# Kernel tuning notes

Measured on AMD Instinct MI355X. Metric: run time of the kernel, lower is better.

Reference implementation:

```python
import jax, jax.numpy as jnp
import numpy as np

EPS = 1e-8

def setup_inputs() -> dict:
    key = jax.random.key(0)
    k1, k2, k3, k4 = jax.random.split(key, 4)
    B, S, K, N = 8, 32, 8192, 8192
    x = jax.random.normal(k1, (B, S, K), dtype=jnp.float32)
    # unpacked AWQ 4-bit weights: int8 values in [-8, 7] (stored as int32 here)
    qweight = jax.random.randint(k2, (K, N), -8, 8, dtype=jnp.int32)
    w_scales = jax.random.uniform(k3, (N,), dtype=jnp.float32) * 0.01 + 1e-4
    bias = jax.random.normal(k4, (N,), dtype=jnp.float32)
    return {"x": x, "qweight": qweight, "w_scales": w_scales, "bias": bias}

def reference(x, qweight, w_scales, bias):
    K = x.shape[-1]
    x2 = x.reshape(-1, K)                                  # [M, K]
    # per-token symmetric int8 activation quantization
    max_abs = jnp.max(jnp.abs(x2), axis=-1, keepdims=True)  # [M, 1]
    act_scales = jnp.maximum(max_abs / 127.0, EPS)
    x_q = jnp.clip(jnp.round(x2 / act_scales), -127, 127).astype(jnp.int8)
    out = x_q.astype(jnp.float32) @ qweight.astype(jnp.float32)  # [M, N]
    # dequant rescale: per-token * per-channel, then bias
    out = out * act_scales * w_scales[None, :] + bias[None, :]
    out = out.reshape(*x.shape[:-1], out.shape[-1])
    return out.astype(x.dtype)
```

## Files before the change

### kernel.cpp

```cpp
#include <hip/hip_runtime.h>

#define M_ 256
#define K_ 8192
#define N_ 8192

typedef int v4i __attribute__((ext_vector_type(4)));
typedef int v16i __attribute__((ext_vector_type(16)));

__global__ __launch_bounds__(256) void awq_quant(const float* __restrict__ x,
                                                 signed char* __restrict__ xqt,
                                                 float* __restrict__ scales) {
    const int m = blockIdx.x;
    const int t = threadIdx.x;
    const float4* xrow = (const float4*)(x + (size_t)m * K_);
    float4 v[8];
    float mx = 0.0f;
#pragma unroll
    for (int j = 0; j < 8; ++j) {
        v[j] = xrow[j * 256 + t];
        mx = fmaxf(mx, fmaxf(fmaxf(fabsf(v[j].x), fabsf(v[j].y)),
                             fmaxf(fabsf(v[j].z), fabsf(v[j].w))));
    }
#pragma unroll
    for (int off = 32; off > 0; off >>= 1) mx = fmaxf(mx, __shfl_xor(mx, off, 64));
    __shared__ float red[4];
    if ((t & 63) == 0) red[t >> 6] = mx;
    __syncthreads();
    mx = fmaxf(fmaxf(red[0], red[1]), fmaxf(red[2], red[3]));
    const float scale = fmaxf(mx / 127.0f, 1e-8f);

    char* base = (char*)xqt + ((size_t)(m >> 5) << 18);
    const int ml = m & 31;
#pragma unroll
    for (int j = 0; j < 8; ++j) {
        const int q0 = (int)fminf(fmaxf(rintf(v[j].x / scale), -127.0f), 127.0f);
        const int q1 = (int)fminf(fmaxf(rintf(v[j].y / scale), -127.0f), 127.0f);
        const int q2 = (int)fminf(fmaxf(rintf(v[j].z / scale), -127.0f), 127.0f);
        const int q3 = (int)fminf(fmaxf(rintf(v[j].w / scale), -127.0f), 127.0f);
        const int packed = (q0 & 255) | ((q1 & 255) << 8) | ((q2 & 255) << 16) | ((q3 & 255) << 24);
        const int k0 = 4 * (j * 256 + t);
        const int addr = ((k0 >> 8) << 13) + (((k0 >> 5) & 7) << 10) +
                         ((ml + (((k0 >> 4) & 1) << 5)) << 4) + (k0 & 15);
        *(int*)(base + addr) = packed;
    }
    if (t == 0) scales[m] = scale;
}


__device__ __forceinline__ void stage_b(char* btn, int bwo,
                                        const int4& w0, const int4& w1,
                                        const int4& w2, const int4& w3) {
    const int* p0 = (const int*)&w0;
    const int* p1 = (const int*)&w1;
    const int* p2 = (const int*)&w2;
    const int* p3 = (const int*)&w3;
#pragma unroll
    for (int j = 0; j < 4; ++j) {
        const unsigned u = __builtin_amdgcn_perm((unsigned)p1[j], (unsigned)p0[j], 0x00000400u);
        const unsigned w = __builtin_amdgcn_perm((unsigned)p3[j], (unsigned)p2[j], 0x00000400u);
        const unsigned o = __builtin_amdgcn_perm(w, u, 0x05040100u);
        *(unsigned*)(btn + bwo + j * 272) = o;
    }
}

__global__ __launch_bounds__(512) void awq_gemm(const signed char* __restrict__ xqt,
                                                const float* __restrict__ scales,
                                                const int* __restrict__ qw,
                                                const float* __restrict__ wscale,
                                                const float* __restrict__ bias,
                                                float* __restrict__ out) {
    __shared__ __align__(16) char btile[2][32 * 272];
    const int t = threadIdx.x;
    const int lane = t & 63;
    const int wave = t >> 6;
    const int n0 = blockIdx.x * 32;

    const int sa = t & 7;
    const int sr = t >> 3;
    const int* qbase = qw + (size_t)(4 * sr) * N_ + n0 + 4 * sa;

    const signed char* xqb = xqt + ((size_t)wave << 18) + lane * 16;

    const int bro = (lane & 31) * 272 + (lane >> 5) * 16;
    const int bwo = (4 * sa) * 272 + 4 * sr;

    v16i acc = {};
    v4i aE[8], aO[8];
    int4 sA[4], sB[4];

    auto loadq = [&](int4* dst, int chunk) {
        const int4* q = (const int4*)(qbase + (size_t)chunk * 256 * N_);
        dst[0] = q[0];
        dst[1] = q[N_ / 4];
        dst[2] = q[2 * (N_ / 4)];
        dst[3] = q[3 * (N_ / 4)];
    };

#pragma unroll
    for (int ks = 0; ks < 8; ++ks) aE[ks] = *(const v4i*)(xqb + ks * 1024);
    loadq(sA, 0);
    loadq(sB, 1);
    stage_b(&btile[0][0], bwo, sA[0], sA[1], sA[2], sA[3]);
    asm volatile("s_waitcnt lgkmcnt(0)" ::: "memory");
    __builtin_amdgcn_s_barrier();
    __builtin_amdgcn_sched_barrier(0);

    for (int sc = 0; sc < 32; sc += 2) {
        {
            const int ra = (sc + 1 < 32) ? sc + 1 : 31;
#pragma unroll
            for (int ks = 0; ks < 8; ++ks)
                aO[ks] = *(const v4i*)(xqb + ra * 8192 + ks * 1024);
            const int c2 = (sc + 2 < 32) ? sc + 2 : 31;
            loadq(sA, c2);
            __builtin_amdgcn_sched_barrier(0);
            const char* btc = &btile[0][0];
#pragma unroll
            for (int ks = 0; ks < 8; ++ks) {
                const v4i bf = *(const v4i*)(btc + bro + ks * 32);
                acc = __builtin_amdgcn_mfma_i32_32x32x32_i8(aE[ks], bf, acc, 0, 0, 0);
            }
            stage_b(&btile[1][0], bwo, sB[0], sB[1], sB[2], sB[3]);
            asm volatile("s_waitcnt lgkmcnt(0)" ::: "memory");
            __builtin_amdgcn_s_barrier();
            __builtin_amdgcn_sched_barrier(0);
        }
        {
            const int ra = (sc + 2 < 32) ? sc + 2 : 31;
#pragma unroll
            for (int ks = 0; ks < 8; ++ks)
                aE[ks] = *(const v4i*)(xqb + ra * 8192 + ks * 1024);
            const int c3 = (sc + 3 < 32) ? sc + 3 : 31;
            loadq(sB, c3);
            __builtin_amdgcn_sched_barrier(0);
            const char* btc = &btile[1][0];
#pragma unroll
            for (int ks = 0; ks < 8; ++ks) {
                const v4i bf = *(const v4i*)(btc + bro + ks * 32);
                acc = __builtin_amdgcn_mfma_i32_32x32x32_i8(aO[ks], bf, acc, 0, 0, 0);
            }
            stage_b(&btile[0][0], bwo, sA[0], sA[1], sA[2], sA[3]);
            asm volatile("s_waitcnt lgkmcnt(0)" ::: "memory");
            __builtin_amdgcn_s_barrier();
            __builtin_amdgcn_sched_barrier(0);
        }
    }

    const int n = n0 + (lane & 31);
    const float wn = wscale[n];
    const float bn = bias[n];
    const int mb = wave * 32 + 4 * (lane >> 5);
#pragma unroll
    for (int g = 0; g < 16; ++g) {
        const int m = mb + (g & 3) + 8 * (g >> 2);
        out[(size_t)m * N_ + n] = ((float)acc[g] * scales[m]) * wn + bn;
    }
}

extern "C" void kernel_launch(void* const* d_in, const int* in_sizes, int n_in,
                              void* d_out, int out_size, void* d_ws, size_t ws_size,
                              hipStream_t stream) {
    const float* x    = (const float*)d_in[0];
    const int*   qw   = (const int*)d_in[1];
    const float* wsc  = (const float*)d_in[2];
    const float* bias = (const float*)d_in[3];
    float* out = (float*)d_out;

    signed char* xqbuf  = (signed char*)d_ws;
    float*       scales = (float*)((char*)d_ws + (size_t)M_ * K_);

    awq_quant<<<M_, 256, 0, stream>>>(x, xqbuf, scales);
    awq_gemm<<<N_ / 32, 512, 0, stream>>>(xqbuf, scales, qw, wsc, bias, out);
}
```

Baseline: 63.92 us.

## Double K-step per barrier and stream A fragments in-place during MFMA loop

Each pipeline stage now covers 512 K values (two chunks) instead of 256, which halves the number of barriers and B-tile staging rounds. The LDS tile grows to 528-byte rows. A fragments go into a single 16-entry register array, and each entry is refilled right after the MFMA that consumes it, instead of alternating between two 8-entry arrays. A launch-bounds occupancy hint of 2 blocks per CU is added, which pushes the compiler to cap register use. The risk is register pressure from the 16 A fragments plus 16 int4 weight values in flight.

```diff
diff --git a/kernel.cpp b/kernel.cpp
--- a/kernel.cpp
+++ b/kernel.cpp
@@ -47,29 +47,30 @@
 }
 
 
-__device__ __forceinline__ void stage_b(char* btn, int bwo,
-                                        const int4& w0, const int4& w1,
-                                        const int4& w2, const int4& w3) {
-    const int* p0 = (const int*)&w0;
-    const int* p1 = (const int*)&w1;
-    const int* p2 = (const int*)&w2;
-    const int* p3 = (const int*)&w3;
+__device__ __forceinline__ void stage_pair(char* btn, int bwo, const int4* w) {
 #pragma unroll
-    for (int j = 0; j < 4; ++j) {
-        const unsigned u = __builtin_amdgcn_perm((unsigned)p1[j], (unsigned)p0[j], 0x00000400u);
-        const unsigned w = __builtin_amdgcn_perm((unsigned)p3[j], (unsigned)p2[j], 0x00000400u);
-        const unsigned o = __builtin_amdgcn_perm(w, u, 0x05040100u);
-        *(unsigned*)(btn + bwo + j * 272) = o;
+    for (int c = 0; c < 2; ++c) {
+        const int* p0 = (const int*)&w[c * 4 + 0];
+        const int* p1 = (const int*)&w[c * 4 + 1];
+        const int* p2 = (const int*)&w[c * 4 + 2];
+        const int* p3 = (const int*)&w[c * 4 + 3];
+#pragma unroll
+        for (int j = 0; j < 4; ++j) {
+            const unsigned u = __builtin_amdgcn_perm((unsigned)p1[j], (unsigned)p0[j], 0x00000400u);
+            const unsigned v = __builtin_amdgcn_perm((unsigned)p3[j], (unsigned)p2[j], 0x00000400u);
+            const unsigned o = __builtin_amdgcn_perm(v, u, 0x05040100u);
+            *(unsigned*)(btn + bwo + c * 256 + j * 528) = o;
+        }
     }
 }
 
-__global__ __launch_bounds__(512) void awq_gemm(const signed char* __restrict__ xqt,
-                                                const float* __restrict__ scales,
-                                                const int* __restrict__ qw,
-                                                const float* __restrict__ wscale,
-                                                const float* __restrict__ bias,
-                                                float* __restrict__ out) {
-    __shared__ __align__(16) char btile[2][32 * 272];
+__global__ __launch_bounds__(512, 2) void awq_gemm(const signed char* __restrict__ xqt,
+                                                   const float* __restrict__ scales,
+                                                   const int* __restrict__ qw,
+                                                   const float* __restrict__ wscale,
+                                                   const float* __restrict__ bias,
+                                                   float* __restrict__ out) {
+    __shared__ __align__(16) char btile[2][32 * 528];
     const int t = threadIdx.x;
     const int lane = t & 63;
     const int wave = t >> 6;
@@ -81,65 +82,63 @@
 
     const signed char* xqb = xqt + ((size_t)wave << 18) + lane * 16;
 
-    const int bro = (lane & 31) * 272 + (lane >> 5) * 16;
-    const int bwo = (4 * sa) * 272 + 4 * sr;
+    const int bro = (lane & 31) * 528 + (lane >> 5) * 16;
+    const int bwo = (4 * sa) * 528 + 4 * sr;
 
     v16i acc = {};
-    v4i aE[8], aO[8];
-    int4 sA[4], sB[4];
+    v4i aF[16];
+    int4 sA[8], sB[8];
 
-    auto loadq = [&](int4* dst, int chunk) {
-        const int4* q = (const int4*)(qbase + (size_t)chunk * 256 * N_);
-        dst[0] = q[0];
-        dst[1] = q[N_ / 4];
-        dst[2] = q[2 * (N_ / 4)];
-        dst[3] = q[3 * (N_ / 4)];
+    auto loadq = [&](int4* dst, int pair) {
+        const int4* q = (const int4*)(qbase + (size_t)pair * 512 * N_);
+#pragma unroll
+        for (int c = 0; c < 2; ++c)
+#pragma unroll
+            for (int i = 0; i < 4; ++i)
+                dst[c * 4 + i] = q[(size_t)(256 * c + i) * (N_ / 4)];
     };
 
-#pragma unroll
-    for (int ks = 0; ks < 8; ++ks) aE[ks] = *(const v4i*)(xqb + ks * 1024);
     loadq(sA, 0);
     loadq(sB, 1);
-    stage_b(&btile[0][0], bwo, sA[0], sA[1], sA[2], sA[3]);
+#pragma unroll
+    for (int f = 0; f < 16; ++f)
+        aF[f] = *(const v4i*)(xqb + (f >> 3) * 8192 + (f & 7) * 1024);
+    stage_pair(&btile[0][0], bwo, sA);
     asm volatile("s_waitcnt lgkmcnt(0)" ::: "memory");
     __builtin_amdgcn_s_barrier();
     __builtin_amdgcn_sched_barrier(0);
 
-    for (int sc = 0; sc < 32; sc += 2) {
+    for (int p = 0; p < 16; p += 2) {
         {
-            const int ra = (sc + 1 < 32) ? sc + 1 : 31;
-#pragma unroll
-            for (int ks = 0; ks < 8; ++ks)
-                aO[ks] = *(const v4i*)(xqb + ra * 8192 + ks * 1024);
-            const int c2 = (sc + 2 < 32) ? sc + 2 : 31;
-            loadq(sA, c2);
+            const int pn = (p + 2 < 16) ? p + 2 : 15;
+            loadq(sA, pn);
             __builtin_amdgcn_sched_barrier(0);
+            const int ra = (p + 1 < 16) ? p + 1 : 15;
             const char* btc = &btile[0][0];
 #pragma unroll
-            for (int ks = 0; ks < 8; ++ks) {
-                const v4i bf = *(const v4i*)(btc + bro + ks * 32);
-                acc = __builtin_amdgcn_mfma_i32_32x32x32_i8(aE[ks], bf, acc, 0, 0, 0);
+            for (int f = 0; f < 16; ++f) {
+                const v4i bf = *(const v4i*)(btc + bro + (f >> 3) * 256 + (f & 7) * 32);
+                acc = __builtin_amdgcn_mfma_i32_32x32x32_i8(aF[f], bf, acc, 0, 0, 0);
+                aF[f] = *(const v4i*)(xqb + (size_t)ra * 16384 + (f >> 3) * 8192 + (f & 7) * 1024);
             }
-            stage_b(&btile[1][0], bwo, sB[0], sB[1], sB[2], sB[3]);
+            stage_pair(&btile[1][0], bwo, sB);
             asm volatile("s_waitcnt lgkmcnt(0)" ::: "memory");
             __builtin_amdgcn_s_barrier();
             __builtin_amdgcn_sched_barrier(0);
         }
         {
-            const int ra = (sc + 2 < 32) ? sc + 2 : 31;
-#pragma unroll
-            for (int ks = 0; ks < 8; ++ks)
-                aE[ks] = *(const v4i*)(xqb + ra * 8192 + ks * 1024);
-            const int c3 = (sc + 3 < 32) ? sc + 3 : 31;
-            loadq(sB, c3);
+            const int pn = (p + 3 < 16) ? p + 3 : 15;
+            loadq(sB, pn);
             __builtin_amdgcn_sched_barrier(0);
+            const int ra = (p + 2 < 16) ? p + 2 : 15;
             const char* btc = &btile[1][0];
 #pragma unroll
-            for (int ks = 0; ks < 8; ++ks) {
-                const v4i bf = *(const v4i*)(btc + bro + ks * 32);
-                acc = __builtin_amdgcn_mfma_i32_32x32x32_i8(aO[ks], bf, acc, 0, 0, 0);
+            for (int f = 0; f < 16; ++f) {
+                const v4i bf = *(const v4i*)(btc + bro + (f >> 3) * 256 + (f & 7) * 32);
+                acc = __builtin_amdgcn_mfma_i32_32x32x32_i8(aF[f], bf, acc, 0, 0, 0);
+                aF[f] = *(const v4i*)(xqb + (size_t)ra * 16384 + (f >> 3) * 8192 + (f & 7) * 1024);
             }
-            stage_b(&btile[0][0], bwo, sA[0], sA[1], sA[2], sA[3]);
+            stage_pair(&btile[0][0], bwo, sA);
             asm volatile("s_waitcnt lgkmcnt(0)" ::: "memory");
             __builtin_amdgcn_s_barrier();
             __builtin_amdgcn_sched_barrier(0);
```

After: 75.67 us. +18.4%, slower.

## Use 64-wide N tiles with split-K over two halves plus reduce kernel

Applied to the files above, without the earlier changes.

Adds a GEMM variant where each block computes a 64-column tile over half of K, with two accumulators per wave so each A fragment feeds two MFMAs. The two K halves are written as fp32 partials to workspace, and a separate elementwise kernel sums them and applies the activation scale, weight scale and bias. The aim is to halve the A-operand reloads per output column and keep 256 blocks to fill the CUs. In exchange it writes and reads two 8 MB partial buffers, adds a third launch, and only runs when the workspace is at least 20 MB, otherwise the old path is used.

```diff
diff --git a/kernel.cpp b/kernel.cpp
--- a/kernel.cpp
+++ b/kernel.cpp
@@ -46,7 +46,6 @@
     if (t == 0) scales[m] = scale;
 }
 
-
 __device__ __forceinline__ void stage_b(char* btn, int bwo,
                                         const int4& w0, const int4& w1,
                                         const int4& w2, const int4& w3) {
@@ -63,39 +62,129 @@
     }
 }
 
-__global__ __launch_bounds__(512) void awq_gemm(const signed char* __restrict__ xqt,
-                                                const float* __restrict__ scales,
-                                                const int* __restrict__ qw,
-                                                const float* __restrict__ wscale,
-                                                const float* __restrict__ bias,
-                                                float* __restrict__ out) {
+__global__ __launch_bounds__(512, 2) void awq_gemm64(const signed char* __restrict__ xqt,
+                                                     const int* __restrict__ qw,
+                                                     float* __restrict__ part) {
+    __shared__ __align__(16) char btile[2][64 * 272];
+    const int t = threadIdx.x;
+    const int lane = t & 63;
+    const int wave = t >> 6;
+    const int bid = blockIdx.x;
+    const int kh = bid & 1;
+    const int n0 = (bid >> 1) * 64;
+
+    const int cg = t & 15;
+    const int q0 = t >> 4;
+    const int* qbase = qw + ((size_t)(kh * 4096 + 4 * q0)) * N_ + n0 + 4 * cg;
+
+    const signed char* xqb = xqt + ((size_t)wave << 18) + lane * 16;
+
+    const int bro0 = (lane & 31) * 272 + (lane >> 5) * 16;
+    const int bro1 = (32 + (lane & 31)) * 272 + (lane >> 5) * 16;
+    const int bwo = (4 * cg) * 272 + 4 * q0;
+
+    v16i acc0 = {}, acc1 = {};
+    v4i aE[8], aO[8];
+    int4 sA[8], sB[8];
+
+    auto loadq = [&](int4* dst, int p) {
+        const int* q = qbase + (size_t)p * 256 * N_;
+#pragma unroll
+        for (int qd = 0; qd < 2; ++qd)
+#pragma unroll
+            for (int i = 0; i < 4; ++i)
+                dst[qd * 4 + i] = *(const int4*)(q + (size_t)(128 * qd + i) * N_);
+    };
+    auto loada = [&](v4i* a, int p) {
+#pragma unroll
+        for (int f = 0; f < 8; ++f)
+            a[f] = *(const v4i*)(xqb + (size_t)(kh * 16 + p) * 8192 + f * 1024);
+    };
+    auto stage64 = [&](char* btn, const int4* w) {
+        stage_b(btn, bwo, w[0], w[1], w[2], w[3]);
+        stage_b(btn, bwo + 128, w[4], w[5], w[6], w[7]);
+    };
+
+    loadq(sA, 0);
+    loadq(sB, 1);
+    loada(aE, 0);
+    stage64(&btile[0][0], sA);
+    asm volatile("s_waitcnt lgkmcnt(0)" ::: "memory");
+    __builtin_amdgcn_s_barrier();
+    __builtin_amdgcn_sched_barrier(0);
+
+    for (int p = 0; p < 16; p += 2) {
+        {
+            loada(aO, (p + 1 < 16) ? p + 1 : 15);
+            loadq(sA, (p + 2 < 16) ? p + 2 : 15);
+            __builtin_amdgcn_sched_barrier(0);
+            const char* btc = &btile[0][0];
+#pragma unroll
+            for (int f = 0; f < 8; ++f) {
+                const v4i b0 = *(const v4i*)(btc + bro0 + f * 32);
+                acc0 = __builtin_amdgcn_mfma_i32_32x32x32_i8(aE[f], b0, acc0, 0, 0, 0);
+                const v4i b1 = *(const v4i*)(btc + bro1 + f * 32);
+                acc1 = __builtin_amdgcn_mfma_i32_32x32x32_i8(aE[f], b1, acc1, 0, 0, 0);
+            }
+            stage64(&btile[1][0], sB);
+            asm volatile("s_waitcnt lgkmcnt(0)" ::: "memory");
+            __builtin_amdgcn_s_barrier();
+            __builtin_amdgcn_sched_barrier(0);
+        }
+        {
+            loada(aE, (p + 2 < 16) ? p + 2 : 15);
+            loadq(sB, (p + 3 < 16) ? p + 3 : 15);
+            __builtin_amdgcn_sched_barrier(0);
+            const char* btc = &btile[1][0];
+#pragma unroll
+            for (int f = 0; f < 8; ++f) {
+                const v4i b0 = *(const v4i*)(btc + bro0 + f * 32);
+                acc0 = __builtin_amdgcn_mfma_i32_32x32x32_i8(aO[f], b0, acc0, 0, 0, 0);
+                const v4i b1 = *(const v4i*)(btc + bro1 + f * 32);
+                acc1 = __builtin_amdgcn_mfma_i32_32x32x32_i8(aO[f], b1, acc1, 0, 0, 0);
+            }
+            stage64(&btile[0][0], sA);
+            asm volatile("s_waitcnt lgkmcnt(0)" ::: "memory");
+            __builtin_amdgcn_s_barrier();
+            __builtin_amdgcn_sched_barrier(0);
+        }
+    }
+
+    float* pb = part + (size_t)kh * M_ * N_;
+    const int mb = wave * 32 + 4 * (lane >> 5);
+#pragma unroll
+    for (int g = 0; g < 16; ++g) {
+        const int m = mb + (g & 3) + 8 * (g >> 2);
+        pb[(size_t)m * N_ + n0 + (lane & 31)]      = (float)acc0[g];
+        pb[(size_t)m * N_ + n0 + 32 + (lane & 31)] = (float)acc1[g];
+    }
+}
+
+__global__ __launch_bounds__(512) void awq_gemm32(const signed char* __restrict__ xqt,
+                                                  const float* __restrict__ scales,
+                                                  const int* __restrict__ qw,
+                                                  const float* __restrict__ wscale,
+                                                  const float* __restrict__ bias,
+                                                  float* __restrict__ out) {
     __shared__ __align__(16) char btile[2][32 * 272];
     const int t = threadIdx.x;
     const int lane = t & 63;
     const int wave = t >> 6;
     const int n0 = blockIdx.x * 32;
-
     const int sa = t & 7;
     const int sr = t >> 3;
     const int* qbase = qw + (size_t)(4 * sr) * N_ + n0 + 4 * sa;
-
     const signed char* xqb = xqt + ((size_t)wave << 18) + lane * 16;
-
     const int bro = (lane & 31) * 272 + (lane >> 5) * 16;
     const int bwo = (4 * sa) * 272 + 4 * sr;
 
     v16i acc = {};
     v4i aE[8], aO[8];
     int4 sA[4], sB[4];
-
     auto loadq = [&](int4* dst, int chunk) {
         const int4* q = (const int4*)(qbase + (size_t)chunk * 256 * N_);
-        dst[0] = q[0];
-        dst[1] = q[N_ / 4];
-        dst[2] = q[2 * (N_ / 4)];
-        dst[3] = q[3 * (N_ / 4)];
-    };
-
+        dst[0] = q[0]; dst[1] = q[N_ / 4]; dst[2] = q[2 * (N_ / 4)]; dst[3] = q[3 * (N_ / 4)];
+    };
 #pragma unroll
     for (int ks = 0; ks < 8; ++ks) aE[ks] = *(const v4i*)(xqb + ks * 1024);
     loadq(sA, 0);
@@ -111,8 +200,7 @@
 #pragma unroll
             for (int ks = 0; ks < 8; ++ks)
                 aO[ks] = *(const v4i*)(xqb + ra * 8192 + ks * 1024);
-            const int c2 = (sc + 2 < 32) ? sc + 2 : 31;
-            loadq(sA, c2);
+            loadq(sA, (sc + 2 < 32) ? sc + 2 : 31);
             __builtin_amdgcn_sched_barrier(0);
             const char* btc = &btile[0][0];
 #pragma unroll
@@ -130,8 +218,7 @@
 #pragma unroll
             for (int ks = 0; ks < 8; ++ks)
                 aE[ks] = *(const v4i*)(xqb + ra * 8192 + ks * 1024);
-            const int c3 = (sc + 3 < 32) ? sc + 3 : 31;
-            loadq(sB, c3);
+            loadq(sB, (sc + 3 < 32) ? sc + 3 : 31);
             __builtin_amdgcn_sched_barrier(0);
             const char* btc = &btile[1][0];
 #pragma unroll
@@ -145,7 +232,6 @@
             __builtin_amdgcn_sched_barrier(0);
         }
     }
-
     const int n = n0 + (lane & 31);
     const float wn = wscale[n];
     const float bn = bias[n];
@@ -155,6 +241,28 @@
         const int m = mb + (g & 3) + 8 * (g >> 2);
         out[(size_t)m * N_ + n] = ((float)acc[g] * scales[m]) * wn + bn;
     }
+}
+
+__global__ __launch_bounds__(256) void awq_reduce(const float* __restrict__ p0,
+                                                  const float* __restrict__ p1,
+                                                  const float* __restrict__ scales,
+                                                  const float* __restrict__ wsc,
+                                                  const float* __restrict__ bias,
+                                                  float* __restrict__ out) {
+    const int idx = blockIdx.x * 256 + threadIdx.x;
+    const float4 a = ((const float4*)p0)[idx];
+    const float4 b = ((const float4*)p1)[idx];
+    const int n4 = (idx * 4) & (N_ - 1);
+    const int m = idx >> 11;
+    const float as = scales[m];
+    const float4 w = *(const float4*)(wsc + n4);
+    const float4 bi = *(const float4*)(bias + n4);
+    float4 o;
+    o.x = ((a.x + b.x) * as) * w.x + bi.x;
+    o.y = ((a.y + b.y) * as) * w.y + bi.y;
+    o.z = ((a.z + b.z) * as) * w.z + bi.z;
+    o.w = ((a.w + b.w) * as) * w.w + bi.w;
+    ((float4*)out)[idx] = o;
 }
 
 extern "C" void kernel_launch(void* const* d_in, const int* in_sizes, int n_in,
@@ -167,8 +275,15 @@
     float* out = (float*)d_out;
 
     signed char* xqbuf  = (signed char*)d_ws;
-    float*       scales = (float*)((char*)d_ws + (size_t)M_ * K_);
+    float*       scales = (float*)((char*)d_ws + (2u << 20));
+    float*       part   = (float*)((char*)d_ws + (4u << 20));
 
     awq_quant<<<M_, 256, 0, stream>>>(x, xqbuf, scales);
-    awq_gemm<<<N_ / 32, 512, 0, stream>>>(xqbuf, scales, qw, wsc, bias, out);
-}
+    if (ws_size >= (20u << 20)) {
+        awq_gemm64<<<256, 512, 0, stream>>>(xqbuf, qw, part);
+        awq_reduce<<<(M_ * N_ / 4) / 256, 256, 0, stream>>>(
+            part, part + (size_t)M_ * N_, scales, wsc, bias, out);
+    } else {
+        awq_gemm32<<<N_ / 32, 512, 0, stream>>>(xqbuf, scales, qw, wsc, bias, out);
+    }
+}
```

Measured after the change: 73.45 us. 14.9% more time.

## Fuse activation quantization and int8 GEMM into one cooperative kernel

Applied to the files above, without the earlier changes.

Merges the per-token quantization kernel and the int8 MFMA GEMM into a single cooperative launch. Each of the 256 blocks quantizes one token row, then a grid-wide sync is followed by the same GEMM tile loop. This removes one kernel launch and the gap between the two kernels. In exchange it adds a grid barrier and the overhead of a cooperative launch, and it falls back to two launches if the cooperative launch fails.

```diff
diff --git a/kernel.cpp b/kernel.cpp
--- a/kernel.cpp
+++ b/kernel.cpp
@@ -1,4 +1,5 @@
 #include <hip/hip_runtime.h>
+#include <hip/hip_cooperative_groups.h>
 
 #define M_ 256
 #define K_ 8192
@@ -6,6 +7,160 @@
 
 typedef int v4i __attribute__((ext_vector_type(4)));
 typedef int v16i __attribute__((ext_vector_type(16)));
+
+namespace cg = cooperative_groups;
+
+
+__device__ __forceinline__ void stage_b(char* btn, int bwo,
+                                        const int4& w0, const int4& w1,
+                                        const int4& w2, const int4& w3) {
+    const int* p0 = (const int*)&w0;
+    const int* p1 = (const int*)&w1;
+    const int* p2 = (const int*)&w2;
+    const int* p3 = (const int*)&w3;
+#pragma unroll
+    for (int j = 0; j < 4; ++j) {
+        const unsigned u = __builtin_amdgcn_perm((unsigned)p1[j], (unsigned)p0[j], 0x00000400u);
+        const unsigned w = __builtin_amdgcn_perm((unsigned)p3[j], (unsigned)p2[j], 0x00000400u);
+        const unsigned o = __builtin_amdgcn_perm(w, u, 0x05040100u);
+        *(unsigned*)(btn + bwo + j * 272) = o;
+    }
+}
+
+__global__ __launch_bounds__(512) void awq_fused(const float* __restrict__ x,
+                                                 signed char* __restrict__ xqt,
+                                                 float* __restrict__ scales,
+                                                 const int* __restrict__ qw,
+                                                 const float* __restrict__ wscale,
+                                                 const float* __restrict__ bias,
+                                                 float* __restrict__ out) {
+    __shared__ __align__(16) char btile[2][32 * 272];
+    __shared__ float red[8];
+    const int t = threadIdx.x;
+    const int bid = blockIdx.x;
+
+    {
+        const int m = bid;
+        const float4* xrow = (const float4*)(x + (size_t)m * K_);
+        float4 v[4];
+        float mx = 0.0f;
+#pragma unroll
+        for (int j = 0; j < 4; ++j) {
+            v[j] = xrow[j * 512 + t];
+            mx = fmaxf(mx, fmaxf(fmaxf(fabsf(v[j].x), fabsf(v[j].y)),
+                                 fmaxf(fabsf(v[j].z), fabsf(v[j].w))));
+        }
+#pragma unroll
+        for (int off = 32; off > 0; off >>= 1) mx = fmaxf(mx, __shfl_xor(mx, off, 64));
+        if ((t & 63) == 0) red[t >> 6] = mx;
+        __syncthreads();
+        mx = fmaxf(fmaxf(fmaxf(red[0], red[1]), fmaxf(red[2], red[3])),
+                   fmaxf(fmaxf(red[4], red[5]), fmaxf(red[6], red[7])));
+        const float scale = fmaxf(mx / 127.0f, 1e-8f);
+
+        char* base = (char*)xqt + ((size_t)(m >> 5) << 18);
+        const int ml = m & 31;
+#pragma unroll
+        for (int j = 0; j < 4; ++j) {
+            const int q0 = (int)fminf(fmaxf(rintf(v[j].x / scale), -127.0f), 127.0f);
+            const int q1 = (int)fminf(fmaxf(rintf(v[j].y / scale), -127.0f), 127.0f);
+            const int q2 = (int)fminf(fmaxf(rintf(v[j].z / scale), -127.0f), 127.0f);
+            const int q3 = (int)fminf(fmaxf(rintf(v[j].w / scale), -127.0f), 127.0f);
+            const int packed = (q0 & 255) | ((q1 & 255) << 8) | ((q2 & 255) << 16) | ((q3 & 255) << 24);
+            const int k0 = 4 * (j * 512 + t);
+            const int addr = ((k0 >> 8) << 13) + (((k0 >> 5) & 7) << 10) +
+                             ((ml + (((k0 >> 4) & 1) << 5)) << 4) + (k0 & 15);
+            *(int*)(base + addr) = packed;
+        }
+        if (t == 0) scales[m] = scale;
+    }
+
+    __threadfence();
+    cg::this_grid().sync();
+
+    const int lane = t & 63;
+    const int wave = t >> 6;
+    const int n0 = bid * 32;
+
+    const int sa = t & 7;
+    const int sr = t >> 3;
+    const int* qbase = qw + (size_t)(4 * sr) * N_ + n0 + 4 * sa;
+
+    const signed char* xqb = xqt + ((size_t)wave << 18) + lane * 16;
+
+    const int bro = (lane & 31) * 272 + (lane >> 5) * 16;
+    const int bwo = (4 * sa) * 272 + 4 * sr;
+
+    v16i acc = {};
+    v4i aE[8], aO[8];
+    int4 sA[4], sB[4];
+
+    auto loadq = [&](int4* dst, int chunk) {
+        const int4* q = (const int4*)(qbase + (size_t)chunk * 256 * N_);
+        dst[0] = q[0];
+        dst[1] = q[N_ / 4];
+        dst[2] = q[2 * (N_ / 4)];
+        dst[3] = q[3 * (N_ / 4)];
+    };
+
+#pragma unroll
+    for (int ks = 0; ks < 8; ++ks) aE[ks] = *(const v4i*)(xqb + ks * 1024);
+    loadq(sA, 0);
+    loadq(sB, 1);
+    stage_b(&btile[0][0], bwo, sA[0], sA[1], sA[2], sA[3]);
+    asm volatile("s_waitcnt lgkmcnt(0)" ::: "memory");
+    __builtin_amdgcn_s_barrier();
+    __builtin_amdgcn_sched_barrier(0);
+
+    for (int sc = 0; sc < 32; sc += 2) {
+        {
+            const int ra = (sc + 1 < 32) ? sc + 1 : 31;
+#pragma unroll
+            for (int ks = 0; ks < 8; ++ks)
+                aO[ks] = *(const v4i*)(xqb + ra * 8192 + ks * 1024);
+            loadq(sA, (sc + 2 < 32) ? sc + 2 : 31);
+            __builtin_amdgcn_sched_barrier(0);
+            const char* btc = &btile[0][0];
+#pragma unroll
+            for (int ks = 0; ks < 8; ++ks) {
+                const v4i bf = *(const v4i*)(btc + bro + ks * 32);
+                acc = __builtin_amdgcn_mfma_i32_32x32x32_i8(aE[ks], bf, acc, 0, 0, 0);
+            }
+            stage_b(&btile[1][0], bwo, sB[0], sB[1], sB[2], sB[3]);
+            asm volatile("s_waitcnt lgkmcnt(0)" ::: "memory");
+            __builtin_amdgcn_s_barrier();
+            __builtin_amdgcn_sched_barrier(0);
+        }
+        {
+            const int ra = (sc + 2 < 32) ? sc + 2 : 31;
+#pragma unroll
+            for (int ks = 0; ks < 8; ++ks)
+                aE[ks] = *(const v4i*)(xqb + ra * 8192 + ks * 1024);
+            loadq(sB, (sc + 3 < 32) ? sc + 3 : 31);
+            __builtin_amdgcn_sched_barrier(0);
+            const char* btc = &btile[1][0];
+#pragma unroll
+            for (int ks = 0; ks < 8; ++ks) {
+                const v4i bf = *(const v4i*)(btc + bro + ks * 32);
+                acc = __builtin_amdgcn_mfma_i32_32x32x32_i8(aO[ks], bf, acc, 0, 0, 0);
+            }
+            stage_b(&btile[0][0], bwo, sA[0], sA[1], sA[2], sA[3]);
+            asm volatile("s_waitcnt lgkmcnt(0)" ::: "memory");
+            __builtin_amdgcn_s_barrier();
+            __builtin_amdgcn_sched_barrier(0);
+        }
+    }
+
+    const int n = n0 + (lane & 31);
+    const float wn = wscale[n];
+    const float bn = bias[n];
+    const int mb = wave * 32 + 4 * (lane >> 5);
+#pragma unroll
+    for (int g = 0; g < 16; ++g) {
+        const int m = mb + (g & 3) + 8 * (g >> 2);
+        out[(size_t)m * N_ + n] = ((float)acc[g] * scales[m]) * wn + bn;
+    }
+}
 
 __global__ __launch_bounds__(256) void awq_quant(const float* __restrict__ x,
                                                  signed char* __restrict__ xqt,
@@ -44,23 +199,6 @@
         *(int*)(base + addr) = packed;
     }
     if (t == 0) scales[m] = scale;
-}
-
-
-__device__ __forceinline__ void stage_b(char* btn, int bwo,
-                                        const int4& w0, const int4& w1,
-                                        const int4& w2, const int4& w3) {
-    const int* p0 = (const int*)&w0;
-    const int* p1 = (const int*)&w1;
-    const int* p2 = (const int*)&w2;
-    const int* p3 = (const int*)&w3;
-#pragma unroll
-    for (int j = 0; j < 4; ++j) {
-        const unsigned u = __builtin_amdgcn_perm((unsigned)p1[j], (unsigned)p0[j], 0x00000400u);
-        const unsigned w = __builtin_amdgcn_perm((unsigned)p3[j], (unsigned)p2[j], 0x00000400u);
-        const unsigned o = __builtin_amdgcn_perm(w, u, 0x05040100u);
-        *(unsigned*)(btn + bwo + j * 272) = o;
-    }
 }
 
 __global__ __launch_bounds__(512) void awq_gemm(const signed char* __restrict__ xqt,
@@ -74,28 +212,20 @@
     const int lane = t & 63;
     const int wave = t >> 6;
     const int n0 = blockIdx.x * 32;
-
     const int sa = t & 7;
     const int sr = t >> 3;
     const int* qbase = qw + (size_t)(4 * sr) * N_ + n0 + 4 * sa;
-
     const signed char* xqb = xqt + ((size_t)wave << 18) + lane * 16;
-
     const int bro = (lane & 31) * 272 + (lane >> 5) * 16;
     const int bwo = (4 * sa) * 272 + 4 * sr;
 
     v16i acc = {};
     v4i aE[8], aO[8];
     int4 sA[4], sB[4];
-
     auto loadq = [&](int4* dst, int chunk) {
         const int4* q = (const int4*)(qbase + (size_t)chunk * 256 * N_);
-        dst[0] = q[0];
-        dst[1] = q[N_ / 4];
-        dst[2] = q[2 * (N_ / 4)];
-        dst[3] = q[3 * (N_ / 4)];
+        dst[0] = q[0]; dst[1] = q[N_ / 4]; dst[2] = q[2 * (N_ / 4)]; dst[3] = q[3 * (N_ / 4)];
     };
-
 #pragma unroll
     for (int ks = 0; ks < 8; ++ks) aE[ks] = *(const v4i*)(xqb + ks * 1024);
     loadq(sA, 0);
@@ -111,8 +241,7 @@
 #pragma unroll
             for (int ks = 0; ks < 8; ++ks)
                 aO[ks] = *(const v4i*)(xqb + ra * 8192 + ks * 1024);
-            const int c2 = (sc + 2 < 32) ? sc + 2 : 31;
-            loadq(sA, c2);
+            loadq(sA, (sc + 2 < 32) ? sc + 2 : 31);
             __builtin_amdgcn_sched_barrier(0);
             const char* btc = &btile[0][0];
 #pragma unroll
@@ -130,8 +259,7 @@
 #pragma unroll
             for (int ks = 0; ks < 8; ++ks)
                 aE[ks] = *(const v4i*)(xqb + ra * 8192 + ks * 1024);
-            const int c3 = (sc + 3 < 32) ? sc + 3 : 31;
-            loadq(sB, c3);
+            loadq(sB, (sc + 3 < 32) ? sc + 3 : 31);
             __builtin_amdgcn_sched_barrier(0);
             const char* btc = &btile[1][0];
 #pragma unroll
@@ -145,7 +273,6 @@
             __builtin_amdgcn_sched_barrier(0);
         }
     }
-
     const int n = n0 + (lane & 31);
     const float wn = wscale[n];
     const float bn = bias[n];
@@ -169,6 +296,13 @@
     signed char* xqbuf  = (signed char*)d_ws;
     float*       scales = (float*)((char*)d_ws + (size_t)M_ * K_);
 
-    awq_quant<<<M_, 256, 0, stream>>>(x, xqbuf, scales);
-    awq_gemm<<<N_ / 32, 512, 0, stream>>>(xqbuf, scales, qw, wsc, bias, out);
-}
+    void* args[] = {(void*)&x, (void*)&xqbuf, (void*)&scales, (void*)&qw,
+                    (void*)&wsc, (void*)&bias, (void*)&out};
+    hipError_t err = hipLaunchCooperativeKernel((const void*)awq_fused,
+                                                dim3(256), dim3(512),
+                                                args, 0, stream);
+    if (err != hipSuccess) {
+        awq_quant<<<M_, 256, 0, stream>>>(x, xqbuf, scales);
+        awq_gemm<<<N_ / 32, 512, 0, stream>>>(xqbuf, scales, qw, wsc, bias, out);
+    }
+}
```

Measured after the change: 145.8 us. 2.28x slower.
